# Kernel tuning notes

Hardware: AMD Instinct MI355X
Metric: run time of the kernel (lower is better)

## Reference

```python
import jax, jax.numpy as jnp
import numpy as np

B, ENC, DEC, H, W = 8, 64, 128, 128, 128
NEG = -1e30  # masked-softmax fill


def _neighbors(x):
    """x: [B,H,W,C] -> [B,H,W,9,C] 3x3 neighborhood gather (zeros at borders)."""
    b, h, w, c = x.shape
    p = jnp.pad(x, ((0, 0), (1, 1), (1, 1), (0, 0)))
    return jnp.stack([p[:, r:r + h, c_:c_ + w, :] for r in range(3) for c_ in range(3)], axis=3)


def _neighbor_mask(h, w):
    """[H,W,9] bool: which of the 9 neighbors are in-bounds per pixel."""
    m = jnp.pad(jnp.ones((h, w), dtype=bool), ((1, 1), (1, 1)))
    return jnp.stack([m[r:r + h, c_:c_ + w] for r in range(3) for c_ in range(3)], axis=2)


def setup_inputs() -> dict:
    key = jax.random.key(0)
    ks = jax.random.split(key, 12)
    s = 0.05
    return {
        "encoder_features": jax.random.normal(ks[0], (B, ENC, H, W), jnp.float32),
        "decoder_features": jax.random.normal(ks[1], (B, DEC, H, W), jnp.float32),
        "W_enc": jax.random.normal(ks[2], (ENC, ENC), jnp.float32) * s,
        "b_enc": jax.random.normal(ks[3], (ENC,), jnp.float32) * s,
        "W_dec": jax.random.normal(ks[4], (DEC, ENC), jnp.float32) * s,
        "b_dec": jax.random.normal(ks[5], (ENC,), jnp.float32) * s,
        "W_agg": jax.random.normal(ks[6], (ENC, 1), jnp.float32) * s,
        "b_agg": jax.random.normal(ks[7], (1,), jnp.float32) * s,
        "W_attn": jax.random.normal(ks[8], (2 * ENC, ENC), jnp.float32) * s,
        "b_attn": jax.random.normal(ks[9], (ENC,), jnp.float32) * s,
        "conv_w": jax.random.normal(ks[10], (3, 3, DEC, ENC), jnp.float32) * s,  # HWIO
        "conv_b": jax.random.normal(ks[11], (ENC,), jnp.float32) * s,
    }


def reference(encoder_features, decoder_features, W_enc, b_enc, W_dec, b_dec,
              W_agg, b_agg, W_attn, b_attn, conv_w, conv_b):
    # NCHW -> NHWC (format_linear)
    enc = jnp.transpose(encoder_features, (0, 2, 3, 1))  # [B,H,W,ENC]
    dec = jnp.transpose(decoder_features, (0, 2, 3, 1))  # [B,H,W,DEC]

    q = dec @ W_dec + b_dec  # [B,H,W,ENC]
    k = enc @ W_enc + b_enc  # [B,H,W,ENC]
    vals = jax.lax.conv_general_dilated(
        dec, conv_w, window_strides=(1, 1), padding='SAME',
        dimension_numbers=('NHWC', 'HWIO', 'NHWC')) + conv_b  # [B,H,W,ENC]

    kn = _neighbors(k)    # [B,H,W,9,ENC]
    en = _neighbors(enc)  # [B,H,W,9,ENC]
    mask = _neighbor_mask(q.shape[1], q.shape[2])  # [H,W,9]

    # per-neighbor additive score: agg_encoder(tanh(query + key)) -> scalar
    scores = jnp.squeeze(jnp.tanh(q[:, :, :, None, :] + kn) @ W_agg, -1) + b_agg  # [B,H,W,9]
    scores = jnp.where(mask, scores, NEG)
    attn_w = jax.nn.softmax(scores, axis=-1)  # softmax over valid neighbors only
    attn_vec = jnp.einsum('bhwn,bhwnc->bhwc', attn_w, en)  # weighted sum of raw encoder feats

    cat = jnp.concatenate([vals, attn_vec], axis=-1)  # [B,H,W,2*ENC]
    out = cat @ W_attn + b_attn
    out = jnp.where(out >= 0, out, 0.2 * out)  # LeakyReLU(0.2)
    return jnp.transpose(out, (0, 3, 1, 2))  # back to NCHW
```

## Files before the change

### kernel.cpp

```cpp
#include <hip/hip_runtime.h>

#define BB 8
#define ENC_C 64
#define DEC_C 128
#define HH 128
#define WW 128

typedef unsigned short ushort_t;
typedef __attribute__((ext_vector_type(8))) short short8;
typedef __attribute__((ext_vector_type(4))) float f32x4;

static __device__ __forceinline__ ushort_t f2bf(float x) {
  unsigned int u = __builtin_bit_cast(unsigned int, x);
  u += 0x7fff + ((u >> 16) & 1);
  return (ushort_t)(u >> 16);
}
static __device__ __forceinline__ float bf2f(ushort_t v) {
  unsigned int u = ((unsigned int)v) << 16;
  return __builtin_bit_cast(float, u);
}

__global__ __launch_bounds__(64) void pack_w_kernel(
    const float* __restrict__ conv_w, const float* __restrict__ W_attn,
    const float* __restrict__ W_dec, const float* __restrict__ W_enc,
    ushort_t* __restrict__ packedC, ushort_t* __restrict__ packedA,
    ushort_t* __restrict__ packedQ, ushort_t* __restrict__ packedK)
{
  const int blk = blockIdx.x;
  const int l = threadIdx.x;
  const float* W;
  ushort_t* dst;
  int bb;
  if (blk < 144) {
    const int kstep = blk >> 2, nf = blk & 3;
    const int tap = kstep >> 2, dstep = kstep & 3;
    const int n = nf * 16 + (l & 15);
    const int dbase = dstep * 32 + (l >> 4) * 8;
    ushort_t v[8];
    #pragma unroll
    for (int j = 0; j < 8; ++j)
      v[j] = f2bf(conv_w[(tap * DEC_C + dbase + j) * 64 + n]);
    ushort_t* d = packedC + (((long)tap * 16 + dstep * 4 + nf) * 64 + l) * 8;
    #pragma unroll
    for (int j = 0; j < 8; ++j) d[j] = v[j];
    return;
  } else if (blk < 160) {
    W = W_attn; dst = packedA; bb = blk - 144;
  } else if (blk < 176) {
    W = W_dec;  dst = packedQ; bb = blk - 160;
  } else {
    W = W_enc;  dst = packedK; bb = blk - 176;
  }
  const int ks = bb >> 2, nf = bb & 3;
  const int n = nf * 16 + (l & 15);
  const int kbase = ks * 32 + (l >> 4) * 8;
  ushort_t v[8];
  #pragma unroll
  for (int j = 0; j < 8; ++j)
    v[j] = f2bf(W[(kbase + j) * 64 + n]);
  ushort_t* d = dst + ((long)bb * 64 + l) * 8;
  #pragma unroll
  for (int j = 0; j < 8; ++j) d[j] = v[j];
}

__global__ __launch_bounds__(256) void prep_kernel(
    const float* __restrict__ enc, const float* __restrict__ dec,
    const ushort_t* __restrict__ packedQ, const ushort_t* __restrict__ packedK,
    const float* __restrict__ b_enc, const float* __restrict__ b_dec,
    ushort_t* __restrict__ q_nhwc, ushort_t* __restrict__ k_nhwc,
    ushort_t* __restrict__ enc_t, ushort_t* __restrict__ dec_t)
{
  __shared__ float smem[WW * 68];
  const int bh = blockIdx.x;
  const int b = bh >> 7, h = bh & 127;
  const int tid = threadIdx.x;
  const int l = tid & 63;
  const int wv = tid >> 6;
  const int pix0 = wv * 32;
  const int col = l & 15, kg = l >> 4;

  #pragma unroll
  for (int i = 0; i < 32; ++i) {
    int idx = tid + i * 256;
    int cc = idx >> 7, wl = idx & 127;
    smem[wl * 68 + cc] = enc[((b * ENC_C + cc) * HH + h) * WW + wl];
  }
  __syncthreads();

  #pragma unroll
  for (int i = 0; i < 32; ++i) {
    int idx = tid + i * 256;
    int wl = idx >> 6, cc = idx & 63;
    enc_t[((long)bh * WW + wl) * 64 + cc] = f2bf(smem[wl * 68 + cc]);
  }

  f32x4 acck[2][4];
  #pragma unroll
  for (int mf = 0; mf < 2; ++mf)
    #pragma unroll
    for (int nf = 0; nf < 4; ++nf)
      acck[mf][nf] = (f32x4){0.f, 0.f, 0.f, 0.f};

  #pragma unroll
  for (int ks = 0; ks < 2; ++ks) {
    short8 afr[2];
    #pragma unroll
    for (int mf = 0; mf < 2; ++mf) {
      const int pix = pix0 + mf * 16 + col;
      const float4* p = (const float4*)&smem[pix * 68 + ks * 32 + kg * 8];
      float4 x0 = p[0], x1 = p[1];
      short8 v;
      v[0] = (short)f2bf(x0.x); v[1] = (short)f2bf(x0.y);
      v[2] = (short)f2bf(x0.z); v[3] = (short)f2bf(x0.w);
      v[4] = (short)f2bf(x1.x); v[5] = (short)f2bf(x1.y);
      v[6] = (short)f2bf(x1.z); v[7] = (short)f2bf(x1.w);
      afr[mf] = v;
    }
    #pragma unroll
    for (int nf = 0; nf < 4; ++nf) {
      const short8 bfr =
          *(const short8*)(packedK + ((long)(ks * 4 + nf) * 64 + l) * 8);
      acck[0][nf] = __builtin_amdgcn_mfma_f32_16x16x32_bf16(
          afr[0], bfr, acck[0][nf], 0, 0, 0);
      acck[1][nf] = __builtin_amdgcn_mfma_f32_16x16x32_bf16(
          afr[1], bfr, acck[1][nf], 0, 0, 0);
    }
  }
  #pragma unroll
  for (int mf = 0; mf < 2; ++mf)
    #pragma unroll
    for (int nf = 0; nf < 4; ++nf)
      #pragma unroll
      for (int r = 0; r < 4; ++r) {
        const int pix = pix0 + mf * 16 + kg * 4 + r;
        const int c = nf * 16 + col;
        k_nhwc[((long)bh * WW + pix) * 64 + c] = f2bf(acck[mf][nf][r] + b_enc[c]);
      }
  __syncthreads();

  f32x4 accq[2][4];
  #pragma unroll
  for (int mf = 0; mf < 2; ++mf)
    #pragma unroll
    for (int nf = 0; nf < 4; ++nf)
      accq[mf][nf] = (f32x4){0.f, 0.f, 0.f, 0.f};

  #pragma unroll
  for (int hf = 0; hf < 2; ++hf) {
    #pragma unroll
    for (int i = 0; i < 32; ++i) {
      int idx = tid + i * 256;
      int cc = idx >> 7, wl = idx & 127;
      smem[wl * 68 + cc] = dec[((b * DEC_C + hf * 64 + cc) * HH + h) * WW + wl];
    }
    __syncthreads();

    #pragma unroll
    for (int i = 0; i < 32; ++i) {
      int idx = tid + i * 256;
      int wl = idx >> 6, cc = idx & 63;
      dec_t[((long)bh * WW + wl) * DEC_C + hf * 64 + cc] =
          f2bf(smem[wl * 68 + cc]);
    }

    #pragma unroll
    for (int ks2 = 0; ks2 < 2; ++ks2) {
      const int ks = hf * 2 + ks2;
      short8 afr[2];
      #pragma unroll
      for (int mf = 0; mf < 2; ++mf) {
        const int pix = pix0 + mf * 16 + col;
        const float4* p = (const float4*)&smem[pix * 68 + ks2 * 32 + kg * 8];
        float4 x0 = p[0], x1 = p[1];
        short8 v;
        v[0] = (short)f2bf(x0.x); v[1] = (short)f2bf(x0.y);
        v[2] = (short)f2bf(x0.z); v[3] = (short)f2bf(x0.w);
        v[4] = (short)f2bf(x1.x); v[5] = (short)f2bf(x1.y);
        v[6] = (short)f2bf(x1.z); v[7] = (short)f2bf(x1.w);
        afr[mf] = v;
      }
      #pragma unroll
      for (int nf = 0; nf < 4; ++nf) {
        const short8 bfr =
            *(const short8*)(packedQ + ((long)(ks * 4 + nf) * 64 + l) * 8);
        accq[0][nf] = __builtin_amdgcn_mfma_f32_16x16x32_bf16(
            afr[0], bfr, accq[0][nf], 0, 0, 0);
        accq[1][nf] = __builtin_amdgcn_mfma_f32_16x16x32_bf16(
            afr[1], bfr, accq[1][nf], 0, 0, 0);
      }
    }
    __syncthreads();
  }

  #pragma unroll
  for (int mf = 0; mf < 2; ++mf)
    #pragma unroll
    for (int nf = 0; nf < 4; ++nf)
      #pragma unroll
      for (int r = 0; r < 4; ++r) {
        const int pix = pix0 + mf * 16 + kg * 4 + r;
        const int c = nf * 16 + col;
        q_nhwc[((long)bh * WW + pix) * 64 + c] = f2bf(accq[mf][nf][r] + b_dec[c]);
      }
}

__global__ __launch_bounds__(256) void attn_kernel(
    const ushort_t* __restrict__ q_nhwc, const ushort_t* __restrict__ k_nhwc,
    const ushort_t* __restrict__ enc_t, const float* __restrict__ W_agg,
    const float* __restrict__ b_agg, ushort_t* __restrict__ att)
{
  const int nwg = gridDim.x;
  const int cpx = nwg >> 3;
  const int bid = blockIdx.x;
  const int swz = (bid & 7) * cpx + (bid >> 3);
  const int t = swz * 256 + threadIdx.x;
  const int pix = t >> 2;
  const int cb = (t & 3) * 16;
  const int h = (pix >> 7) & 127;
  const int w = pix & 127;

  int off[9]; bool valid[9];
  #pragma unroll
  for (int n = 0; n < 9; ++n) {
    const int dh = n / 3 - 1, dw = n % 3 - 1;
    const int nh = h + dh, nw = w + dw;
    valid[n] = (nh >= 0 && nh < HH && nw >= 0 && nw < WW);
    const int nhc = min(max(nh, 0), HH - 1);
    const int nwc = min(max(nw, 0), WW - 1);
    off[n] = (pix & ~16383) + nhc * WW + nwc;
  }

  const short8* qp = (const short8*)(q_nhwc + ((long)pix << 6) + cb);
  const short8 qa = qp[0], qb = qp[1];

  float wa[16];
  {
    float4 w0 = *(const float4*)(W_agg + cb);
    float4 w1 = *(const float4*)(W_agg + cb + 4);
    float4 w2 = *(const float4*)(W_agg + cb + 8);
    float4 w3 = *(const float4*)(W_agg + cb + 12);
    wa[0]=w0.x; wa[1]=w0.y; wa[2]=w0.z; wa[3]=w0.w;
    wa[4]=w1.x; wa[5]=w1.y; wa[6]=w1.z; wa[7]=w1.w;
    wa[8]=w2.x; wa[9]=w2.y; wa[10]=w2.z; wa[11]=w2.w;
    wa[12]=w3.x; wa[13]=w3.y; wa[14]=w3.z; wa[15]=w3.w;
  }

  float s[9];
  #pragma unroll
  for (int n = 0; n < 9; ++n) {
    const short8* kp = (const short8*)(k_nhwc + ((long)off[n] << 6) + cb);
    const short8 ka = kp[0], kb = kp[1];
    float sc = 0.f;
    #pragma unroll
    for (int e = 0; e < 8; ++e) {
      float x = bf2f((ushort_t)qa[e]) + bf2f((ushort_t)ka[e]);
      x = fminf(fmaxf(x, -15.f), 15.f);
      float z = __builtin_amdgcn_exp2f(x * 2.88539008f);
      float tt = __builtin_fmaf(-2.f, __builtin_amdgcn_rcpf(z + 1.f), 1.f);
      sc = __builtin_fmaf(tt, wa[e], sc);
    }
    #pragma unroll
    for (int e = 0; e < 8; ++e) {
      float x = bf2f((ushort_t)qb[e]) + bf2f((ushort_t)kb[e]);
      x = fminf(fmaxf(x, -15.f), 15.f);
      float z = __builtin_amdgcn_exp2f(x * 2.88539008f);
      float tt = __builtin_fmaf(-2.f, __builtin_amdgcn_rcpf(z + 1.f), 1.f);
      sc = __builtin_fmaf(tt, wa[8 + e], sc);
    }
    s[n] = sc;
  }

  #pragma unroll
  for (int n = 0; n < 9; ++n) {
    s[n] += __shfl_xor(s[n], 1);
    s[n] += __shfl_xor(s[n], 2);
  }

  const float bagg = b_agg[0];
  float m = -1e30f;
  #pragma unroll
  for (int n = 0; n < 9; ++n) {
    s[n] = valid[n] ? (s[n] + bagg) : -1e30f;
    m = fmaxf(m, s[n]);
  }
  float attw[9]; float denom = 0.f;
  #pragma unroll
  for (int n = 0; n < 9; ++n) {
    attw[n] = __builtin_amdgcn_exp2f((s[n] - m) * 1.44269504f);
    denom += attw[n];
  }
  const float inv = __builtin_amdgcn_rcpf(denom);
  #pragma unroll
  for (int n = 0; n < 9; ++n) attw[n] *= inv;

  float a16[16];
  #pragma unroll
  for (int e = 0; e < 16; ++e) a16[e] = 0.f;
  #pragma unroll
  for (int n = 0; n < 9; ++n) {
    const short8* ep = (const short8*)(enc_t + ((long)off[n] << 6) + cb);
    const short8 ea = ep[0], eb = ep[1];
    #pragma unroll
    for (int e = 0; e < 8; ++e)
      a16[e] = __builtin_fmaf(attw[n], bf2f((ushort_t)ea[e]), a16[e]);
    #pragma unroll
    for (int e = 0; e < 8; ++e)
      a16[8 + e] = __builtin_fmaf(attw[n], bf2f((ushort_t)eb[e]), a16[8 + e]);
  }
  short8 o0, o1;
  #pragma unroll
  for (int e = 0; e < 8; ++e) {
    o0[e] = (short)f2bf(a16[e]);
    o1[e] = (short)f2bf(a16[8 + e]);
  }
  short8* op = (short8*)(att + ((long)pix << 6) + cb);
  op[0] = o0;
  op[1] = o1;
}

__global__ __launch_bounds__(256) void conv_out_kernel(
    const ushort_t* __restrict__ dec_t, const ushort_t* __restrict__ packedC,
    const float* __restrict__ conv_b, const ushort_t* __restrict__ attn_nhwc,
    const ushort_t* __restrict__ packedA, const float* __restrict__ b_attn,
    float* __restrict__ out)
{
  __shared__ ushort_t bsh[16384];
  ushort_t* vlds = bsh;
  const int nwg = gridDim.x;
  const int cpx = nwg >> 3;
  const int bid = blockIdx.x;
  const int bh = (bid & 7) * cpx + (bid >> 3);
  const int b = bh >> 7, h = bh & 127;
  const int tid = threadIdx.x;
  const int l = tid & 63;
  const int wv = tid >> 6;
  const int pix0 = wv * 32;
  const int col = l & 15, kg = l >> 4;

  auto stage = [&](int tap) {
    const ushort_t* src = packedC + (long)tap * 8192;
    ushort_t* dstb = bsh + (tap & 1) * 8192 + (long)(tid & ~63) * 8;
    #pragma unroll
    for (int i = 0; i < 4; ++i) {
      __builtin_amdgcn_global_load_lds(
          (const __attribute__((address_space(1))) void*)(src + (long)(i * 256 + tid) * 8),
          (__attribute__((address_space(3))) void*)(dstb + i * 256 * 8),
          16, 0, 0);
    }
  };

  f32x4 acc[2][4];
  #pragma unroll
  for (int mf = 0; mf < 2; ++mf)
    #pragma unroll
    for (int nf = 0; nf < 4; ++nf)
      acc[mf][nf] = (f32x4){0.f, 0.f, 0.f, 0.f};

  stage(0);

  #pragma unroll
  for (int p = 0; p < 9; ++p) {
    __syncthreads();
    if (p + 1 < 9) stage(p + 1);
    const int kh = p / 3, kw = p % 3;
    const int hh = h + kh - 1;
    if (hh >= 0 && hh < HH) {
      const ushort_t* arow = dec_t + ((long)(b * HH + hh) * WW) * DEC_C;
      const ushort_t* bbase = bsh + (p & 1) * 8192;
      short8 afr[4][2];
      #pragma unroll
      for (int ds = 0; ds < 4; ++ds)
        #pragma unroll
        for (int mf = 0; mf < 2; ++mf) {
          const int wp = pix0 + mf * 16 + col + kw - 1;
          short8 z = {0, 0, 0, 0, 0, 0, 0, 0};
          afr[ds][mf] = (wp >= 0 && wp < WW)
              ? *(const short8*)(arow + (long)wp * DEC_C + ds * 32 + kg * 8) : z;
        }
      #pragma unroll
      for (int ds = 0; ds < 4; ++ds)
        #pragma unroll
        for (int nf = 0; nf < 4; ++nf) {
          const short8 bfr =
              *(const short8*)(bbase + ((ds * 4 + nf) * 64 + l) * 8);
          acc[0][nf] = __builtin_amdgcn_mfma_f32_16x16x32_bf16(
              afr[ds][0], bfr, acc[0][nf], 0, 0, 0);
          acc[1][nf] = __builtin_amdgcn_mfma_f32_16x16x32_bf16(
              afr[ds][1], bfr, acc[1][nf], 0, 0, 0);
        }
    }
  }

  __syncthreads();
  #pragma unroll
  for (int mf = 0; mf < 2; ++mf)
    #pragma unroll
    for (int nf = 0; nf < 4; ++nf)
      #pragma unroll
      for (int r = 0; r < 4; ++r) {
        const int pix = pix0 + mf * 16 + kg * 4 + r;
        const int c = nf * 16 + col;
        vlds[pix * 72 + c] = f2bf(acc[mf][nf][r] + conv_b[c]);
      }
  __syncthreads();

  f32x4 ao[4][2];
  #pragma unroll
  for (int mf = 0; mf < 4; ++mf)
    #pragma unroll
    for (int pf = 0; pf < 2; ++pf)
      ao[mf][pf] = (f32x4){0.f, 0.f, 0.f, 0.f};

  #pragma unroll
  for (int ks = 0; ks < 4; ++ks) {
    short8 bfr[2];
    #pragma unroll
    for (int pf = 0; pf < 2; ++pf) {
      const int pix = pix0 + pf * 16 + col;
      short8 v;
      if (ks < 2) {
        v = *(const short8*)&vlds[pix * 72 + ks * 32 + kg * 8];
      } else {
        v = *(const short8*)(attn_nhwc + ((long)bh * WW + pix) * 64 +
                             (ks - 2) * 32 + kg * 8);
      }
      bfr[pf] = v;
    }
    #pragma unroll
    for (int mf = 0; mf < 4; ++mf) {
      const short8 afr =
          *(const short8*)(packedA + ((long)(ks * 4 + mf) * 64 + l) * 8);
      #pragma unroll
      for (int pf = 0; pf < 2; ++pf)
        ao[mf][pf] = __builtin_amdgcn_mfma_f32_16x16x32_bf16(
            afr, bfr[pf], ao[mf][pf], 0, 0, 0);
    }
  }

  #pragma unroll
  for (int mf = 0; mf < 4; ++mf)
    #pragma unroll
    for (int pf = 0; pf < 2; ++pf)
      #pragma unroll
      for (int r = 0; r < 4; ++r) {
        const int n = mf * 16 + kg * 4 + r;
        const int pix = pix0 + pf * 16 + col;
        float o = ao[mf][pf][r] + b_attn[n];
        o = (o >= 0.f) ? o : 0.2f * o;
        out[((long)(b * ENC_C + n) * HH + h) * WW + pix] = o;
      }
}

extern "C" void kernel_launch(void* const* d_in, const int* in_sizes, int n_in,
                              void* d_out, int out_size, void* d_ws, size_t ws_size,
                              hipStream_t stream) {
  const float* enc    = (const float*)d_in[0];
  const float* dec    = (const float*)d_in[1];
  const float* W_enc  = (const float*)d_in[2];
  const float* b_enc  = (const float*)d_in[3];
  const float* W_dec  = (const float*)d_in[4];
  const float* b_dec  = (const float*)d_in[5];
  const float* W_agg  = (const float*)d_in[6];
  const float* b_agg  = (const float*)d_in[7];
  const float* W_attn = (const float*)d_in[8];
  const float* b_attn = (const float*)d_in[9];
  const float* conv_w = (const float*)d_in[10];
  const float* conv_b = (const float*)d_in[11];
  float* out = (float*)d_out;

  const long npix = (long)BB * HH * WW;
  ushort_t* q_bf    = (ushort_t*)d_ws;
  ushort_t* k_bf    = q_bf + npix * 64;
  ushort_t* enc_t   = k_bf + npix * 64;
  ushort_t* dec_t   = enc_t + npix * 64;
  ushort_t* att     = dec_t + npix * 128;
  ushort_t* packedC = att + npix * 64;
  ushort_t* packedA = packedC + 144 * 64 * 8;
  ushort_t* packedQ = packedA + 16 * 64 * 8;
  ushort_t* packedK = packedQ + 16 * 64 * 8;

  hipLaunchKernelGGL(pack_w_kernel, dim3(184), dim3(64), 0, stream,
                     conv_w, W_attn, W_dec, W_enc, packedC, packedA, packedQ, packedK);
  hipLaunchKernelGGL(prep_kernel, dim3(BB * HH), dim3(256), 0, stream,
                     enc, dec, packedQ, packedK, b_enc, b_dec, q_bf, k_bf, enc_t, dec_t);
  hipLaunchKernelGGL(attn_kernel, dim3((int)(npix * 4 / 256)), dim3(256), 0, stream,
                     q_bf, k_bf, enc_t, W_agg, b_agg, att);
  hipLaunchKernelGGL(conv_out_kernel, dim3(BB * HH), dim3(256), 0, stream,
                     dec_t, packedC, conv_b, att, packedA, b_attn, out);
}
```

Baseline: 120.5 us.

## Fuse neighborhood attention into conv/output kernel via LDS staging

Merges the separate attention kernel into the conv+output-projection kernel. Each block computes the attention vectors for its image row (two threads per pixel, 32 channels each) and writes them to a new LDS buffer, which the final MFMA projection then reads instead of a global intermediate. This removes one kernel launch and the global write and re-read of the attention tensor. In exchange it adds LDS use per block, which can lower occupancy, and puts the attention work ahead of the conv loop, overlapped only with the first weight-stage load.

```diff
diff --git a/kernel.cpp b/kernel.cpp
--- a/kernel.cpp
+++ b/kernel.cpp
@@ -204,127 +204,17 @@
       }
 }
 
-__global__ __launch_bounds__(256) void attn_kernel(
+__global__ __launch_bounds__(256) void fused_kernel(
+    const ushort_t* __restrict__ dec_t, const ushort_t* __restrict__ packedC,
+    const float* __restrict__ conv_b,
     const ushort_t* __restrict__ q_nhwc, const ushort_t* __restrict__ k_nhwc,
     const ushort_t* __restrict__ enc_t, const float* __restrict__ W_agg,
-    const float* __restrict__ b_agg, ushort_t* __restrict__ att)
-{
-  const int nwg = gridDim.x;
-  const int cpx = nwg >> 3;
-  const int bid = blockIdx.x;
-  const int swz = (bid & 7) * cpx + (bid >> 3);
-  const int t = swz * 256 + threadIdx.x;
-  const int pix = t >> 2;
-  const int cb = (t & 3) * 16;
-  const int h = (pix >> 7) & 127;
-  const int w = pix & 127;
-
-  int off[9]; bool valid[9];
-  #pragma unroll
-  for (int n = 0; n < 9; ++n) {
-    const int dh = n / 3 - 1, dw = n % 3 - 1;
-    const int nh = h + dh, nw = w + dw;
-    valid[n] = (nh >= 0 && nh < HH && nw >= 0 && nw < WW);
-    const int nhc = min(max(nh, 0), HH - 1);
-    const int nwc = min(max(nw, 0), WW - 1);
-    off[n] = (pix & ~16383) + nhc * WW + nwc;
-  }
-
-  const short8* qp = (const short8*)(q_nhwc + ((long)pix << 6) + cb);
-  const short8 qa = qp[0], qb = qp[1];
-
-  float wa[16];
-  {
-    float4 w0 = *(const float4*)(W_agg + cb);
-    float4 w1 = *(const float4*)(W_agg + cb + 4);
-    float4 w2 = *(const float4*)(W_agg + cb + 8);
-    float4 w3 = *(const float4*)(W_agg + cb + 12);
-    wa[0]=w0.x; wa[1]=w0.y; wa[2]=w0.z; wa[3]=w0.w;
-    wa[4]=w1.x; wa[5]=w1.y; wa[6]=w1.z; wa[7]=w1.w;
-    wa[8]=w2.x; wa[9]=w2.y; wa[10]=w2.z; wa[11]=w2.w;
-    wa[12]=w3.x; wa[13]=w3.y; wa[14]=w3.z; wa[15]=w3.w;
-  }
-
-  float s[9];
-  #pragma unroll
-  for (int n = 0; n < 9; ++n) {
-    const short8* kp = (const short8*)(k_nhwc + ((long)off[n] << 6) + cb);
-    const short8 ka = kp[0], kb = kp[1];
-    float sc = 0.f;
-    #pragma unroll
-    for (int e = 0; e < 8; ++e) {
-      float x = bf2f((ushort_t)qa[e]) + bf2f((ushort_t)ka[e]);
-      x = fminf(fmaxf(x, -15.f), 15.f);
-      float z = __builtin_amdgcn_exp2f(x * 2.88539008f);
-      float tt = __builtin_fmaf(-2.f, __builtin_amdgcn_rcpf(z + 1.f), 1.f);
-      sc = __builtin_fmaf(tt, wa[e], sc);
-    }
-    #pragma unroll
-    for (int e = 0; e < 8; ++e) {
-      float x = bf2f((ushort_t)qb[e]) + bf2f((ushort_t)kb[e]);
-      x = fminf(fmaxf(x, -15.f), 15.f);
-      float z = __builtin_amdgcn_exp2f(x * 2.88539008f);
-      float tt = __builtin_fmaf(-2.f, __builtin_amdgcn_rcpf(z + 1.f), 1.f);
-      sc = __builtin_fmaf(tt, wa[8 + e], sc);
-    }
-    s[n] = sc;
-  }
-
-  #pragma unroll
-  for (int n = 0; n < 9; ++n) {
-    s[n] += __shfl_xor(s[n], 1);
-    s[n] += __shfl_xor(s[n], 2);
-  }
-
-  const float bagg = b_agg[0];
-  float m = -1e30f;
-  #pragma unroll
-  for (int n = 0; n < 9; ++n) {
-    s[n] = valid[n] ? (s[n] + bagg) : -1e30f;
-    m = fmaxf(m, s[n]);
-  }
-  float attw[9]; float denom = 0.f;
-  #pragma unroll
-  for (int n = 0; n < 9; ++n) {
-    attw[n] = __builtin_amdgcn_exp2f((s[n] - m) * 1.44269504f);
-    denom += attw[n];
-  }
-  const float inv = __builtin_amdgcn_rcpf(denom);
-  #pragma unroll
-  for (int n = 0; n < 9; ++n) attw[n] *= inv;
-
-  float a16[16];
-  #pragma unroll
-  for (int e = 0; e < 16; ++e) a16[e] = 0.f;
-  #pragma unroll
-  for (int n = 0; n < 9; ++n) {
-    const short8* ep = (const short8*)(enc_t + ((long)off[n] << 6) + cb);
-    const short8 ea = ep[0], eb = ep[1];
-    #pragma unroll
-    for (int e = 0; e < 8; ++e)
-      a16[e] = __builtin_fmaf(attw[n], bf2f((ushort_t)ea[e]), a16[e]);
-    #pragma unroll
-    for (int e = 0; e < 8; ++e)
-      a16[8 + e] = __builtin_fmaf(attw[n], bf2f((ushort_t)eb[e]), a16[8 + e]);
-  }
-  short8 o0, o1;
-  #pragma unroll
-  for (int e = 0; e < 8; ++e) {
-    o0[e] = (short)f2bf(a16[e]);
-    o1[e] = (short)f2bf(a16[8 + e]);
-  }
-  short8* op = (short8*)(att + ((long)pix << 6) + cb);
-  op[0] = o0;
-  op[1] = o1;
-}
-
-__global__ __launch_bounds__(256) void conv_out_kernel(
-    const ushort_t* __restrict__ dec_t, const ushort_t* __restrict__ packedC,
-    const float* __restrict__ conv_b, const ushort_t* __restrict__ attn_nhwc,
+    const float* __restrict__ b_agg,
     const ushort_t* __restrict__ packedA, const float* __restrict__ b_attn,
     float* __restrict__ out)
 {
   __shared__ ushort_t bsh[16384];
+  __shared__ ushort_t att_lds[WW * 72];
   ushort_t* vlds = bsh;
   const int nwg = gridDim.x;
   const int cpx = nwg >> 3;
@@ -349,14 +239,117 @@
     }
   };
 
+  stage(0);
+
+  {
+    const int w = tid >> 1;
+    const int cb = (tid & 1) * 32;
+
+    int off[9]; bool valid[9];
+    #pragma unroll
+    for (int n = 0; n < 9; ++n) {
+      const int dh = n / 3 - 1, dw = n % 3 - 1;
+      const int nh = h + dh, nw = w + dw;
+      valid[n] = (nh >= 0 && nh < HH && nw >= 0 && nw < WW);
+      const int nhc = min(max(nh, 0), HH - 1);
+      const int nwc = min(max(nw, 0), WW - 1);
+      off[n] = (b * HH + nhc) * WW + nwc;
+    }
+
+    const short8* qp = (const short8*)(q_nhwc + (((long)bh * WW + w) << 6) + cb);
+    const short8 q0 = qp[0], q1 = qp[1], q2 = qp[2], q3 = qp[3];
+
+    float s[9];
+    #pragma unroll
+    for (int n = 0; n < 9; ++n) s[n] = 0.f;
+
+    #pragma unroll
+    for (int c16 = 0; c16 < 2; ++c16) {
+      float wa[16];
+      #pragma unroll
+      for (int e = 0; e < 16; ++e) wa[e] = W_agg[cb + c16 * 16 + e];
+      const short8 qa = (c16 == 0) ? q0 : q2;
+      const short8 qb = (c16 == 0) ? q1 : q3;
+      #pragma unroll
+      for (int n = 0; n < 9; ++n) {
+        const short8* kp =
+            (const short8*)(k_nhwc + (((long)off[n]) << 6) + cb + c16 * 16);
+        const short8 ka = kp[0], kb = kp[1];
+        float sc = 0.f;
+        #pragma unroll
+        for (int e = 0; e < 8; ++e) {
+          float x = bf2f((ushort_t)qa[e]) + bf2f((ushort_t)ka[e]);
+          x = fminf(fmaxf(x, -15.f), 15.f);
+          float z = __builtin_amdgcn_exp2f(x * 2.88539008f);
+          float tt = __builtin_fmaf(-2.f, __builtin_amdgcn_rcpf(z + 1.f), 1.f);
+          sc = __builtin_fmaf(tt, wa[e], sc);
+        }
+        #pragma unroll
+        for (int e = 0; e < 8; ++e) {
+          float x = bf2f((ushort_t)qb[e]) + bf2f((ushort_t)kb[e]);
+          x = fminf(fmaxf(x, -15.f), 15.f);
+          float z = __builtin_amdgcn_exp2f(x * 2.88539008f);
+          float tt = __builtin_fmaf(-2.f, __builtin_amdgcn_rcpf(z + 1.f), 1.f);
+          sc = __builtin_fmaf(tt, wa[8 + e], sc);
+        }
+        s[n] += sc;
+      }
+    }
+
+    #pragma unroll
+    for (int n = 0; n < 9; ++n) s[n] += __shfl_xor(s[n], 1);
+
+    const float bagg = b_agg[0];
+    float m = -1e30f;
+    #pragma unroll
+    for (int n = 0; n < 9; ++n) {
+      s[n] = valid[n] ? (s[n] + bagg) : -1e30f;
+      m = fmaxf(m, s[n]);
+    }
+    float attw[9]; float denom = 0.f;
+    #pragma unroll
+    for (int n = 0; n < 9; ++n) {
+      attw[n] = __builtin_amdgcn_exp2f((s[n] - m) * 1.44269504f);
+      denom += attw[n];
+    }
+    const float inv = __builtin_amdgcn_rcpf(denom);
+    #pragma unroll
+    for (int n = 0; n < 9; ++n) attw[n] *= inv;
+
+    #pragma unroll
+    for (int c16 = 0; c16 < 2; ++c16) {
+      float a16[16];
+      #pragma unroll
+      for (int e = 0; e < 16; ++e) a16[e] = 0.f;
+      #pragma unroll
+      for (int n = 0; n < 9; ++n) {
+        const short8* ep =
+            (const short8*)(enc_t + (((long)off[n]) << 6) + cb + c16 * 16);
+        const short8 ea = ep[0], eb = ep[1];
+        #pragma unroll
+        for (int e = 0; e < 8; ++e)
+          a16[e] = __builtin_fmaf(attw[n], bf2f((ushort_t)ea[e]), a16[e]);
+        #pragma unroll
+        for (int e = 0; e < 8; ++e)
+          a16[8 + e] = __builtin_fmaf(attw[n], bf2f((ushort_t)eb[e]), a16[8 + e]);
+      }
+      short8 o0, o1;
+      #pragma unroll
+      for (int e = 0; e < 8; ++e) {
+        o0[e] = (short)f2bf(a16[e]);
+        o1[e] = (short)f2bf(a16[8 + e]);
+      }
+      *(short8*)&att_lds[w * 72 + cb + c16 * 16]     = o0;
+      *(short8*)&att_lds[w * 72 + cb + c16 * 16 + 8] = o1;
+    }
+  }
+
   f32x4 acc[2][4];
   #pragma unroll
   for (int mf = 0; mf < 2; ++mf)
     #pragma unroll
     for (int nf = 0; nf < 4; ++nf)
       acc[mf][nf] = (f32x4){0.f, 0.f, 0.f, 0.f};
-
-  stage(0);
 
   #pragma unroll
   for (int p = 0; p < 9; ++p) {
@@ -421,8 +414,7 @@
       if (ks < 2) {
         v = *(const short8*)&vlds[pix * 72 + ks * 32 + kg * 8];
       } else {
-        v = *(const short8*)(attn_nhwc + ((long)bh * WW + pix) * 64 +
-                             (ks - 2) * 32 + kg * 8);
+        v = *(const short8*)&att_lds[pix * 72 + (ks - 2) * 32 + kg * 8];
       }
       bfr[pf] = v;
     }
@@ -473,8 +465,7 @@
   ushort_t* k_bf    = q_bf + npix * 64;
   ushort_t* enc_t   = k_bf + npix * 64;
   ushort_t* dec_t   = enc_t + npix * 64;
-  ushort_t* att     = dec_t + npix * 128;
-  ushort_t* packedC = att + npix * 64;
+  ushort_t* packedC = dec_t + npix * 128;
   ushort_t* packedA = packedC + 144 * 64 * 8;
   ushort_t* packedQ = packedA + 16 * 64 * 8;
   ushort_t* packedK = packedQ + 16 * 64 * 8;
@@ -483,8 +474,7 @@
                      conv_w, W_attn, W_dec, W_enc, packedC, packedA, packedQ, packedK);
   hipLaunchKernelGGL(prep_kernel, dim3(BB * HH), dim3(256), 0, stream,
                      enc, dec, packedQ, packedK, b_enc, b_dec, q_bf, k_bf, enc_t, dec_t);
-  hipLaunchKernelGGL(attn_kernel, dim3((int)(npix * 4 / 256)), dim3(256), 0, stream,
-                     q_bf, k_bf, enc_t, W_agg, b_agg, att);
-  hipLaunchKernelGGL(conv_out_kernel, dim3(BB * HH), dim3(256), 0, stream,
-                     dec_t, packedC, conv_b, att, packedA, b_attn, out);
-}
+  hipLaunchKernelGGL(fused_kernel, dim3(BB * HH), dim3(256), 0, stream,
+                     dec_t, packedC, conv_b, q_bf, k_bf, enc_t, W_agg, b_agg,
+                     packedA, b_attn, out);
+}
```

Measured after the change: 123.4 us. +2.4%, slower.

## Split conv_out rows into half-row blocks and read conv weights directly from global

Applied to the files above, without the earlier changes.

The fused conv+output kernel now launches twice as many workgroups, each handling half an image row with 16 pixels per wave instead of 32. The double-buffered LDS staging of conv weights through global_load_lds and its per-tap barriers are removed. Weights are now read directly from global memory or cache for every MFMA, and the A fragments for all three kw taps are loaded per kh row. This adds parallelism and cuts LDS use and synchronisation, but each weight fragment is reused by only one M-fragment instead of two, which raises global and cache traffic per MFMA.

```diff
diff --git a/kernel.cpp b/kernel.cpp
--- a/kernel.cpp
+++ b/kernel.cpp
@@ -324,131 +324,100 @@
     const ushort_t* __restrict__ packedA, const float* __restrict__ b_attn,
     float* __restrict__ out)
 {
-  __shared__ ushort_t bsh[16384];
-  ushort_t* vlds = bsh;
+  __shared__ ushort_t vlds[64 * 72];
   const int nwg = gridDim.x;
   const int cpx = nwg >> 3;
   const int bid = blockIdx.x;
-  const int bh = (bid & 7) * cpx + (bid >> 3);
-  const int b = bh >> 7, h = bh & 127;
+  const int grp = (bid & 7) * cpx + (bid >> 3);
+  const int b = grp >> 8;
+  const int h = (grp & 255) >> 1;
+  const int half = grp & 1;
   const int tid = threadIdx.x;
   const int l = tid & 63;
   const int wv = tid >> 6;
-  const int pix0 = wv * 32;
+  const int pix0 = half * 64 + wv * 16;
   const int col = l & 15, kg = l >> 4;
 
-  auto stage = [&](int tap) {
-    const ushort_t* src = packedC + (long)tap * 8192;
-    ushort_t* dstb = bsh + (tap & 1) * 8192 + (long)(tid & ~63) * 8;
-    #pragma unroll
-    for (int i = 0; i < 4; ++i) {
-      __builtin_amdgcn_global_load_lds(
-          (const __attribute__((address_space(1))) void*)(src + (long)(i * 256 + tid) * 8),
-          (__attribute__((address_space(3))) void*)(dstb + i * 256 * 8),
-          16, 0, 0);
-    }
-  };
-
-  f32x4 acc[2][4];
-  #pragma unroll
-  for (int mf = 0; mf < 2; ++mf)
-    #pragma unroll
-    for (int nf = 0; nf < 4; ++nf)
-      acc[mf][nf] = (f32x4){0.f, 0.f, 0.f, 0.f};
-
-  stage(0);
-
-  #pragma unroll
-  for (int p = 0; p < 9; ++p) {
-    __syncthreads();
-    if (p + 1 < 9) stage(p + 1);
-    const int kh = p / 3, kw = p % 3;
+  f32x4 acc[4];
+  #pragma unroll
+  for (int nf = 0; nf < 4; ++nf) acc[nf] = (f32x4){0.f, 0.f, 0.f, 0.f};
+
+  #pragma unroll 1
+  for (int kh = 0; kh < 3; ++kh) {
     const int hh = h + kh - 1;
-    if (hh >= 0 && hh < HH) {
-      const ushort_t* arow = dec_t + ((long)(b * HH + hh) * WW) * DEC_C;
-      const ushort_t* bbase = bsh + (p & 1) * 8192;
-      short8 afr[4][2];
-      #pragma unroll
-      for (int ds = 0; ds < 4; ++ds)
-        #pragma unroll
-        for (int mf = 0; mf < 2; ++mf) {
-          const int wp = pix0 + mf * 16 + col + kw - 1;
-          short8 z = {0, 0, 0, 0, 0, 0, 0, 0};
-          afr[ds][mf] = (wp >= 0 && wp < WW)
-              ? *(const short8*)(arow + (long)wp * DEC_C + ds * 32 + kg * 8) : z;
-        }
+    if (hh < 0 || hh >= HH) continue;
+    const ushort_t* arow = dec_t + ((long)(b * HH + hh) * WW) * DEC_C;
+
+    short8 afr[3][4];
+    #pragma unroll
+    for (int kw = 0; kw < 3; ++kw) {
+      const int wp = pix0 + col + kw - 1;
+      const bool ok = (wp >= 0 && wp < WW);
+      #pragma unroll
+      for (int ds = 0; ds < 4; ++ds) {
+        short8 z = {0, 0, 0, 0, 0, 0, 0, 0};
+        afr[kw][ds] = ok
+            ? *(const short8*)(arow + (long)wp * DEC_C + ds * 32 + kg * 8) : z;
+      }
+    }
+    #pragma unroll
+    for (int kw = 0; kw < 3; ++kw) {
+      const int tap = kh * 3 + kw;
       #pragma unroll
       for (int ds = 0; ds < 4; ++ds)
         #pragma unroll
         for (int nf = 0; nf < 4; ++nf) {
-          const short8 bfr =
-              *(const short8*)(bbase + ((ds * 4 + nf) * 64 + l) * 8);
-          acc[0][nf] = __builtin_amdgcn_mfma_f32_16x16x32_bf16(
-              afr[ds][0], bfr, acc[0][nf], 0, 0, 0);
-          acc[1][nf] = __builtin_amdgcn_mfma_f32_16x16x32_bf16(
-              afr[ds][1], bfr, acc[1][nf], 0, 0, 0);
+          const short8 bfr = *(const short8*)(
+              packedC + (((long)tap * 16 + ds * 4 + nf) * 64 + l) * 8);
+          acc[nf] = __builtin_amdgcn_mfma_f32_16x16x32_bf16(
+              afr[kw][ds], bfr, acc[nf], 0, 0, 0);
         }
     }
   }
 
+  #pragma unroll
+  for (int nf = 0; nf < 4; ++nf)
+    #pragma unroll
+    for (int r = 0; r < 4; ++r) {
+      const int lp = wv * 16 + kg * 4 + r;
+      const int c = nf * 16 + col;
+      vlds[lp * 72 + c] = f2bf(acc[nf][r] + conv_b[c]);
+    }
   __syncthreads();
-  #pragma unroll
-  for (int mf = 0; mf < 2; ++mf)
-    #pragma unroll
-    for (int nf = 0; nf < 4; ++nf)
-      #pragma unroll
-      for (int r = 0; r < 4; ++r) {
-        const int pix = pix0 + mf * 16 + kg * 4 + r;
-        const int c = nf * 16 + col;
-        vlds[pix * 72 + c] = f2bf(acc[mf][nf][r] + conv_b[c]);
-      }
-  __syncthreads();
-
-  f32x4 ao[4][2];
-  #pragma unroll
-  for (int mf = 0; mf < 4; ++mf)
-    #pragma unroll
-    for (int pf = 0; pf < 2; ++pf)
-      ao[mf][pf] = (f32x4){0.f, 0.f, 0.f, 0.f};
+
+  f32x4 ao[4];
+  #pragma unroll
+  for (int mf = 0; mf < 4; ++mf) ao[mf] = (f32x4){0.f, 0.f, 0.f, 0.f};
 
   #pragma unroll
   for (int ks = 0; ks < 4; ++ks) {
-    short8 bfr[2];
-    #pragma unroll
-    for (int pf = 0; pf < 2; ++pf) {
-      const int pix = pix0 + pf * 16 + col;
-      short8 v;
-      if (ks < 2) {
-        v = *(const short8*)&vlds[pix * 72 + ks * 32 + kg * 8];
-      } else {
-        v = *(const short8*)(attn_nhwc + ((long)bh * WW + pix) * 64 +
-                             (ks - 2) * 32 + kg * 8);
-      }
-      bfr[pf] = v;
+    short8 bfr;
+    if (ks < 2) {
+      bfr = *(const short8*)&vlds[(wv * 16 + col) * 72 + ks * 32 + kg * 8];
+    } else {
+      bfr = *(const short8*)(attn_nhwc +
+                            (((long)(b * HH + h) * WW) + pix0 + col) * 64 +
+                            (ks - 2) * 32 + kg * 8);
     }
     #pragma unroll
     for (int mf = 0; mf < 4; ++mf) {
       const short8 afr =
           *(const short8*)(packedA + ((long)(ks * 4 + mf) * 64 + l) * 8);
-      #pragma unroll
-      for (int pf = 0; pf < 2; ++pf)
-        ao[mf][pf] = __builtin_amdgcn_mfma_f32_16x16x32_bf16(
-            afr, bfr[pf], ao[mf][pf], 0, 0, 0);
+      ao[mf] = __builtin_amdgcn_mfma_f32_16x16x32_bf16(
+          afr, bfr, ao[mf], 0, 0, 0);
     }
   }
 
   #pragma unroll
   for (int mf = 0; mf < 4; ++mf)
     #pragma unroll
-    for (int pf = 0; pf < 2; ++pf)
-      #pragma unroll
-      for (int r = 0; r < 4; ++r) {
-        const int n = mf * 16 + kg * 4 + r;
-        const int pix = pix0 + pf * 16 + col;
-        float o = ao[mf][pf][r] + b_attn[n];
-        o = (o >= 0.f) ? o : 0.2f * o;
-        out[((long)(b * ENC_C + n) * HH + h) * WW + pix] = o;
-      }
+    for (int r = 0; r < 4; ++r) {
+      const int n = mf * 16 + kg * 4 + r;
+      const int pix = pix0 + col;
+      float o = ao[mf][r] + b_attn[n];
+      o = (o >= 0.f) ? o : 0.2f * o;
+      out[((long)(b * ENC_C + n) * HH + h) * WW + pix] = o;
+    }
 }
 
 extern "C" void kernel_launch(void* const* d_in, const int* in_sizes, int n_in,
@@ -485,6 +454,6 @@
                      enc, dec, packedQ, packedK, b_enc, b_dec, q_bf, k_bf, enc_t, dec_t);
   hipLaunchKernelGGL(attn_kernel, dim3((int)(npix * 4 / 256)), dim3(256), 0, stream,
                      q_bf, k_bf, enc_t, W_agg, b_agg, att);
-  hipLaunchKernelGGL(conv_out_kernel, dim3(BB * HH), dim3(256), 0, stream,
+  hipLaunchKernelGGL(conv_out_kernel, dim3(BB * HH * 2), dim3(256), 0, stream,
                      dec_t, packedC, conv_b, att, packedA, b_attn, out);
 }
```

Result: slower. 160.5 us (+33.2%).

## Fold output projection into conv weights and encoder features algebraically

Applied to the files above, without the earlier changes.

Precomputes conv_w·W_attn[:64] as combined conv weights and folds conv_b into a total bias, so the conv kernel directly produces projected output. The attention half of W_attn is applied to encoder features in prep (encw = enc·W_attn[64:]), since the attention-weighted sum is linear, so the attention kernel outputs already-projected values. This removes the second GEMM and LDS round-trip in the final kernel, at the cost of an extra MFMA pass in prep and a per-call weight pre-multiply in pack_w. It also changes where bf16 rounding happens.

```diff
diff --git a/kernel.cpp b/kernel.cpp
--- a/kernel.cpp
+++ b/kernel.cpp
@@ -8,6 +8,7 @@
 
 typedef unsigned short ushort_t;
 typedef __attribute__((ext_vector_type(8))) short short8;
+typedef __attribute__((ext_vector_type(4))) short short4v;
 typedef __attribute__((ext_vector_type(4))) float f32x4;
 
 static __device__ __forceinline__ ushort_t f2bf(float x) {
@@ -23,37 +24,54 @@
 __global__ __launch_bounds__(64) void pack_w_kernel(
     const float* __restrict__ conv_w, const float* __restrict__ W_attn,
     const float* __restrict__ W_dec, const float* __restrict__ W_enc,
-    ushort_t* __restrict__ packedC, ushort_t* __restrict__ packedA,
-    ushort_t* __restrict__ packedQ, ushort_t* __restrict__ packedK)
+    const float* __restrict__ conv_b, const float* __restrict__ b_attn,
+    ushort_t* __restrict__ packedC2, ushort_t* __restrict__ packedW2,
+    ushort_t* __restrict__ packedQ, ushort_t* __restrict__ packedK,
+    float* __restrict__ bias_total)
 {
   const int blk = blockIdx.x;
   const int l = threadIdx.x;
-  const float* W;
-  ushort_t* dst;
-  int bb;
+
   if (blk < 144) {
     const int kstep = blk >> 2, nf = blk & 3;
     const int tap = kstep >> 2, dstep = kstep & 3;
     const int n = nf * 16 + (l & 15);
     const int dbase = dstep * 32 + (l >> 4) * 8;
+    float wcol[64];
+    #pragma unroll
+    for (int c = 0; c < 64; ++c) wcol[c] = W_attn[c * 64 + n];
     ushort_t v[8];
     #pragma unroll
-    for (int j = 0; j < 8; ++j)
-      v[j] = f2bf(conv_w[(tap * DEC_C + dbase + j) * 64 + n]);
-    ushort_t* d = packedC + (((long)tap * 16 + dstep * 4 + nf) * 64 + l) * 8;
+    for (int j = 0; j < 8; ++j) {
+      const float* cw = conv_w + ((long)(tap * DEC_C + dbase + j)) * 64;
+      float acc = 0.f;
+      #pragma unroll
+      for (int c = 0; c < 64; ++c) acc = __builtin_fmaf(cw[c], wcol[c], acc);
+      v[j] = f2bf(acc);
+    }
+    ushort_t* d = packedC2 + (((long)tap * 16 + dstep * 4 + nf) * 64 + l) * 8;
     #pragma unroll
     for (int j = 0; j < 8; ++j) d[j] = v[j];
     return;
-  } else if (blk < 160) {
-    W = W_attn; dst = packedA; bb = blk - 144;
-  } else if (blk < 176) {
-    W = W_dec;  dst = packedQ; bb = blk - 160;
-  } else {
-    W = W_enc;  dst = packedK; bb = blk - 176;
-  }
+  }
+  if (blk == 176) {
+    float acc = b_attn[l];
+    #pragma unroll
+    for (int c = 0; c < 64; ++c)
+      acc = __builtin_fmaf(conv_b[c], W_attn[c * 64 + l], acc);
+    bias_total[l] = acc;
+    return;
+  }
+
+  const float* W;
+  ushort_t* dst;
+  int bb, krow0;
+  if (blk < 152)      { W = W_attn; dst = packedW2; bb = blk - 144; krow0 = 64; }
+  else if (blk < 168) { W = W_dec;  dst = packedQ;  bb = blk - 152; krow0 = 0; }
+  else                { W = W_enc;  dst = packedK;  bb = blk - 168; krow0 = 0; }
   const int ks = bb >> 2, nf = bb & 3;
   const int n = nf * 16 + (l & 15);
-  const int kbase = ks * 32 + (l >> 4) * 8;
+  const int kbase = krow0 + ks * 32 + (l >> 4) * 8;
   ushort_t v[8];
   #pragma unroll
   for (int j = 0; j < 8; ++j)
@@ -66,9 +84,10 @@
 __global__ __launch_bounds__(256) void prep_kernel(
     const float* __restrict__ enc, const float* __restrict__ dec,
     const ushort_t* __restrict__ packedQ, const ushort_t* __restrict__ packedK,
+    const ushort_t* __restrict__ packedW2,
     const float* __restrict__ b_enc, const float* __restrict__ b_dec,
     ushort_t* __restrict__ q_nhwc, ushort_t* __restrict__ k_nhwc,
-    ushort_t* __restrict__ enc_t, ushort_t* __restrict__ dec_t)
+    ushort_t* __restrict__ encw, ushort_t* __restrict__ dec_t)
 {
   __shared__ float smem[WW * 68];
   const int bh = blockIdx.x;
@@ -87,19 +106,14 @@
   }
   __syncthreads();
 
-  #pragma unroll
-  for (int i = 0; i < 32; ++i) {
-    int idx = tid + i * 256;
-    int wl = idx >> 6, cc = idx & 63;
-    enc_t[((long)bh * WW + wl) * 64 + cc] = f2bf(smem[wl * 68 + cc]);
-  }
-
-  f32x4 acck[2][4];
+  f32x4 acck[2][4], accw[2][4];
   #pragma unroll
   for (int mf = 0; mf < 2; ++mf)
     #pragma unroll
-    for (int nf = 0; nf < 4; ++nf)
+    for (int nf = 0; nf < 4; ++nf) {
       acck[mf][nf] = (f32x4){0.f, 0.f, 0.f, 0.f};
+      accw[mf][nf] = (f32x4){0.f, 0.f, 0.f, 0.f};
+    }
 
   #pragma unroll
   for (int ks = 0; ks < 2; ++ks) {
@@ -118,12 +132,17 @@
     }
     #pragma unroll
     for (int nf = 0; nf < 4; ++nf) {
-      const short8 bfr =
+      const short8 bk =
           *(const short8*)(packedK + ((long)(ks * 4 + nf) * 64 + l) * 8);
-      acck[0][nf] = __builtin_amdgcn_mfma_f32_16x16x32_bf16(
-          afr[0], bfr, acck[0][nf], 0, 0, 0);
-      acck[1][nf] = __builtin_amdgcn_mfma_f32_16x16x32_bf16(
-          afr[1], bfr, acck[1][nf], 0, 0, 0);
+      const short8 bw =
+          *(const short8*)(packedW2 + ((long)(ks * 4 + nf) * 64 + l) * 8);
+      #pragma unroll
+      for (int mf = 0; mf < 2; ++mf) {
+        acck[mf][nf] = __builtin_amdgcn_mfma_f32_16x16x32_bf16(
+            afr[mf], bk, acck[mf][nf], 0, 0, 0);
+        accw[mf][nf] = __builtin_amdgcn_mfma_f32_16x16x32_bf16(
+            afr[mf], bw, accw[mf][nf], 0, 0, 0);
+      }
     }
   }
   #pragma unroll
@@ -135,6 +154,7 @@
         const int pix = pix0 + mf * 16 + kg * 4 + r;
         const int c = nf * 16 + col;
         k_nhwc[((long)bh * WW + pix) * 64 + c] = f2bf(acck[mf][nf][r] + b_enc[c]);
+        encw[((long)bh * WW + pix) * 64 + c]   = f2bf(accw[mf][nf][r]);
       }
   __syncthreads();
 
@@ -206,8 +226,8 @@
 
 __global__ __launch_bounds__(256) void attn_kernel(
     const ushort_t* __restrict__ q_nhwc, const ushort_t* __restrict__ k_nhwc,
-    const ushort_t* __restrict__ enc_t, const float* __restrict__ W_agg,
-    const float* __restrict__ b_agg, ushort_t* __restrict__ att)
+    const ushort_t* __restrict__ encw, const float* __restrict__ W_agg,
+    const float* __restrict__ b_agg, ushort_t* __restrict__ attw2)
 {
   const int nwg = gridDim.x;
   const int cpx = nwg >> 3;
@@ -298,7 +318,7 @@
   for (int e = 0; e < 16; ++e) a16[e] = 0.f;
   #pragma unroll
   for (int n = 0; n < 9; ++n) {
-    const short8* ep = (const short8*)(enc_t + ((long)off[n] << 6) + cb);
+    const short8* ep = (const short8*)(encw + ((long)off[n] << 6) + cb);
     const short8 ea = ep[0], eb = ep[1];
     #pragma unroll
     for (int e = 0; e < 8; ++e)
@@ -313,19 +333,17 @@
     o0[e] = (short)f2bf(a16[e]);
     o1[e] = (short)f2bf(a16[8 + e]);
   }
-  short8* op = (short8*)(att + ((long)pix << 6) + cb);
+  short8* op = (short8*)(attw2 + ((long)pix << 6) + cb);
   op[0] = o0;
   op[1] = o1;
 }
 
-__global__ __launch_bounds__(256) void conv_out_kernel(
-    const ushort_t* __restrict__ dec_t, const ushort_t* __restrict__ packedC,
-    const float* __restrict__ conv_b, const ushort_t* __restrict__ attn_nhwc,
-    const ushort_t* __restrict__ packedA, const float* __restrict__ b_attn,
+__global__ __launch_bounds__(256) void conv2_kernel(
+    const ushort_t* __restrict__ dec_t, const ushort_t* __restrict__ packedC2,
+    const ushort_t* __restrict__ attw2, const float* __restrict__ bias_total,
     float* __restrict__ out)
 {
   __shared__ ushort_t bsh[16384];
-  ushort_t* vlds = bsh;
   const int nwg = gridDim.x;
   const int cpx = nwg >> 3;
   const int bid = blockIdx.x;
@@ -338,7 +356,7 @@
   const int col = l & 15, kg = l >> 4;
 
   auto stage = [&](int tap) {
-    const ushort_t* src = packedC + (long)tap * 8192;
+    const ushort_t* src = packedC2 + (long)tap * 8192;
     ushort_t* dstb = bsh + (tap & 1) * 8192 + (long)(tid & ~63) * 8;
     #pragma unroll
     for (int i = 0; i < 4; ++i) {
@@ -349,12 +367,12 @@
     }
   };
 
-  f32x4 acc[2][4];
-  #pragma unroll
-  for (int mf = 0; mf < 2; ++mf)
-    #pragma unroll
-    for (int nf = 0; nf < 4; ++nf)
-      acc[mf][nf] = (f32x4){0.f, 0.f, 0.f, 0.f};
+  f32x4 acc[4][2];
+  #pragma unroll
+  for (int mf = 0; mf < 4; ++mf)
+    #pragma unroll
+    for (int pf = 0; pf < 2; ++pf)
+      acc[mf][pf] = (f32x4){0.f, 0.f, 0.f, 0.f};
 
   stage(0);
 
@@ -367,88 +385,47 @@
     if (hh >= 0 && hh < HH) {
       const ushort_t* arow = dec_t + ((long)(b * HH + hh) * WW) * DEC_C;
       const ushort_t* bbase = bsh + (p & 1) * 8192;
-      short8 afr[4][2];
+      short8 pfr[4][2];
+      #pragma unroll
+      for (int pf = 0; pf < 2; ++pf) {
+        const int wp = pix0 + pf * 16 + col + kw - 1;
+        const bool ok = (wp >= 0 && wp < WW);
+        #pragma unroll
+        for (int ds = 0; ds < 4; ++ds) {
+          short8 z = {0, 0, 0, 0, 0, 0, 0, 0};
+          pfr[ds][pf] = ok
+              ? *(const short8*)(arow + (long)wp * DEC_C + ds * 32 + kg * 8) : z;
+        }
+      }
       #pragma unroll
       for (int ds = 0; ds < 4; ++ds)
         #pragma unroll
-        for (int mf = 0; mf < 2; ++mf) {
-          const int wp = pix0 + mf * 16 + col + kw - 1;
-          short8 z = {0, 0, 0, 0, 0, 0, 0, 0};
-          afr[ds][mf] = (wp >= 0 && wp < WW)
-              ? *(const short8*)(arow + (long)wp * DEC_C + ds * 32 + kg * 8) : z;
+        for (int mf = 0; mf < 4; ++mf) {
+          const short8 wfr =
+              *(const short8*)(bbase + ((ds * 4 + mf) * 64 + l) * 8);
+          acc[mf][0] = __builtin_amdgcn_mfma_f32_16x16x32_bf16(
+              wfr, pfr[ds][0], acc[mf][0], 0, 0, 0);
+          acc[mf][1] = __builtin_amdgcn_mfma_f32_16x16x32_bf16(
+              wfr, pfr[ds][1], acc[mf][1], 0, 0, 0);
         }
-      #pragma unroll
-      for (int ds = 0; ds < 4; ++ds)
-        #pragma unroll
-        for (int nf = 0; nf < 4; ++nf) {
-          const short8 bfr =
-              *(const short8*)(bbase + ((ds * 4 + nf) * 64 + l) * 8);
-          acc[0][nf] = __builtin_amdgcn_mfma_f32_16x16x32_bf16(
-              afr[ds][0], bfr, acc[0][nf], 0, 0, 0);
-          acc[1][nf] = __builtin_amdgcn_mfma_f32_16x16x32_bf16(
-              afr[ds][1], bfr, acc[1][nf], 0, 0, 0);
-        }
-    }
-  }
-
-  __syncthreads();
-  #pragma unroll
-  for (int mf = 0; mf < 2; ++mf)
-    #pragma unroll
-    for (int nf = 0; nf < 4; ++nf)
-      #pragma unroll
-      for (int r = 0; r < 4; ++r) {
-        const int pix = pix0 + mf * 16 + kg * 4 + r;
-        const int c = nf * 16 + col;
-        vlds[pix * 72 + c] = f2bf(acc[mf][nf][r] + conv_b[c]);
-      }
-  __syncthreads();
-
-  f32x4 ao[4][2];
+    }
+  }
+
   #pragma unroll
   for (int mf = 0; mf < 4; ++mf)
-    #pragma unroll
-    for (int pf = 0; pf < 2; ++pf)
-      ao[mf][pf] = (f32x4){0.f, 0.f, 0.f, 0.f};
-
-  #pragma unroll
-  for (int ks = 0; ks < 4; ++ks) {
-    short8 bfr[2];
     #pragma unroll
     for (int pf = 0; pf < 2; ++pf) {
       const int pix = pix0 + pf * 16 + col;
-      short8 v;
-      if (ks < 2) {
-        v = *(const short8*)&vlds[pix * 72 + ks * 32 + kg * 8];
-      } else {
-        v = *(const short8*)(attn_nhwc + ((long)bh * WW + pix) * 64 +
-                             (ks - 2) * 32 + kg * 8);
-      }
-      bfr[pf] = v;
-    }
-    #pragma unroll
-    for (int mf = 0; mf < 4; ++mf) {
-      const short8 afr =
-          *(const short8*)(packedA + ((long)(ks * 4 + mf) * 64 + l) * 8);
-      #pragma unroll
-      for (int pf = 0; pf < 2; ++pf)
-        ao[mf][pf] = __builtin_amdgcn_mfma_f32_16x16x32_bf16(
-            afr, bfr[pf], ao[mf][pf], 0, 0, 0);
-    }
-  }
-
-  #pragma unroll
-  for (int mf = 0; mf < 4; ++mf)
-    #pragma unroll
-    for (int pf = 0; pf < 2; ++pf)
+      const short4v av = *(const short4v*)(
+          attw2 + ((long)bh * WW + pix) * 64 + mf * 16 + kg * 4);
       #pragma unroll
       for (int r = 0; r < 4; ++r) {
-        const int n = mf * 16 + kg * 4 + r;
-        const int pix = pix0 + pf * 16 + col;
-        float o = ao[mf][pf][r] + b_attn[n];
+        const int ch = mf * 16 + kg * 4 + r;
+        float o = acc[mf][pf][r] + bf2f((ushort_t)av[r]) + bias_total[ch];
         o = (o >= 0.f) ? o : 0.2f * o;
-        out[((long)(b * ENC_C + n) * HH + h) * WW + pix] = o;
-      }
+        out[((long)(b * ENC_C + ch) * HH + h) * WW + pix] = o;
+      }
+    }
 }
 
 extern "C" void kernel_launch(void* const* d_in, const int* in_sizes, int n_in,
@@ -469,22 +446,25 @@
   float* out = (float*)d_out;
 
   const long npix = (long)BB * HH * WW;
-  ushort_t* q_bf    = (ushort_t*)d_ws;
-  ushort_t* k_bf    = q_bf + npix * 64;
-  ushort_t* enc_t   = k_bf + npix * 64;
-  ushort_t* dec_t   = enc_t + npix * 64;
-  ushort_t* att     = dec_t + npix * 128;
-  ushort_t* packedC = att + npix * 64;
-  ushort_t* packedA = packedC + 144 * 64 * 8;
-  ushort_t* packedQ = packedA + 16 * 64 * 8;
-  ushort_t* packedK = packedQ + 16 * 64 * 8;
-
-  hipLaunchKernelGGL(pack_w_kernel, dim3(184), dim3(64), 0, stream,
-                     conv_w, W_attn, W_dec, W_enc, packedC, packedA, packedQ, packedK);
+  ushort_t* q_bf     = (ushort_t*)d_ws;
+  ushort_t* k_bf     = q_bf + npix * 64;
+  ushort_t* encw     = k_bf + npix * 64;
+  ushort_t* dec_t    = encw + npix * 64;
+  ushort_t* attw2    = dec_t + npix * 128;
+  ushort_t* packedC2 = attw2 + npix * 64;
+  ushort_t* packedW2 = packedC2 + 144 * 64 * 8;
+  ushort_t* packedQ  = packedW2 + 8 * 64 * 8;
+  ushort_t* packedK  = packedQ + 16 * 64 * 8;
+  float* bias_total  = (float*)(packedK + 8 * 64 * 8);
+
+  hipLaunchKernelGGL(pack_w_kernel, dim3(177), dim3(64), 0, stream,
+                     conv_w, W_attn, W_dec, W_enc, conv_b, b_attn,
+                     packedC2, packedW2, packedQ, packedK, bias_total);
   hipLaunchKernelGGL(prep_kernel, dim3(BB * HH), dim3(256), 0, stream,
-                     enc, dec, packedQ, packedK, b_enc, b_dec, q_bf, k_bf, enc_t, dec_t);
+                     enc, dec, packedQ, packedK, packedW2, b_enc, b_dec,
+                     q_bf, k_bf, encw, dec_t);
   hipLaunchKernelGGL(attn_kernel, dim3((int)(npix * 4 / 256)), dim3(256), 0, stream,
-                     q_bf, k_bf, enc_t, W_agg, b_agg, att);
-  hipLaunchKernelGGL(conv_out_kernel, dim3(BB * HH), dim3(256), 0, stream,
-                     dec_t, packedC, conv_b, att, packedA, b_attn, out);
-}
+                     q_bf, k_bf, encw, W_agg, b_agg, attw2);
+  hipLaunchKernelGGL(conv2_kernel, dim3(BB * HH), dim3(256), 0, stream,
+                     dec_t, packedC2, attw2, bias_total, out);
+}
```

Result: slower. 136.4 us (+13.2%).
